# Performance work log

Measured on AMD Instinct MI355X. Metric: run time of the kernel, lower is better.

The kernel has to match this reference:

```python
import jax, jax.numpy as jnp
import numpy as np

B, T, H = 1024, 512, 128
TIMESTEPS_PREDICT = 4


def setup_inputs() -> dict:
    key = jax.random.key(0)
    ks = jax.random.split(key, 7)
    s = 1.0 / np.sqrt(H)
    return {
        "x": jax.random.normal(ks[0], (B, T, 1), jnp.float32),
        "hidden": jnp.zeros((B, H), jnp.float32),
        "fc0_w": jax.random.normal(ks[1], (H, 1), jnp.float32) * s,
        "fc0_b": jax.random.normal(ks[2], (H,), jnp.float32) * 0.1,
        "fc_w": jax.random.normal(ks[3], (H, H), jnp.float32) * s,
        "fc_b": jax.random.normal(ks[4], (H,), jnp.float32) * 0.1,
        "dec_w": jax.random.normal(ks[5], (1, H), jnp.float32) * s,
        "dec_b": jax.random.normal(ks[6], (1,), jnp.float32) * 0.1,
    }


def _rnn(x, h, fc0_w, fc0_b, fc_w, fc_b):
    """Vanilla tanh RNN over time. x: (B, Tx, 1), h: (B, H) -> (ys (B, Tx, H), h)."""
    def step(h, xt):  # xt: (B, 1)
        h = jnp.tanh(xt @ fc0_w.T + fc0_b + h @ fc_w.T + fc_b)
        return h, h
    h, ys = jax.lax.scan(step, h, jnp.swapaxes(x, 0, 1))  # ys: (Tx, B, H)
    return jnp.swapaxes(ys, 0, 1), h


def reference(x, hidden, fc0_w, fc0_b, fc_w, fc_b, dec_w, dec_b):
    out, h = _rnn(x, hidden, fc0_w, fc0_b, fc_w, fc_b)  # (B, T, H)
    y = out @ dec_w.T + dec_b  # (B, T, 1)
    last = y[:, -1:, :]  # (B, 1, 1)
    for _ in range(TIMESTEPS_PREDICT):
        out_h, h = _rnn(last, h, fc0_w, fc0_b, fc_w, fc_b)
        last = out_h @ dec_w.T + dec_b
        y = jnp.concatenate([y, last], axis=1)
    return y  # (B, T + TIMESTEPS_PREDICT, 1)
```

## Files before the change

### kernel.cpp

```cpp
#include <hip/hip_runtime.h>
#include <hip/hip_bf16.h>


#define BB 1024
#define TT 512
#define HH 128
#define TOUT 516
#define BM 16
#define XSTR 513
#define YSTR 517
#define PQS 36
#define TWOLOG2E 2.885390082f

typedef __attribute__((ext_vector_type(8))) _Float16 f16x8;
typedef __attribute__((ext_vector_type(4))) float f32x4;

#define MFMA16(A_, B_, C_) __builtin_amdgcn_mfma_f32_16x16x32_f16(A_, B_, C_, 0, 0, 0)

__global__ void detect_dtype(const void* w, int* flag) {
    const int lane = threadIdx.x;
    const __hip_bfloat16* p = (const __hip_bfloat16*)w;
    const float v0 = __bfloat162float(p[lane]);
    const float v1 = __bfloat162float(p[64 + lane]);
    const bool bad = !(fabsf(v0) < 100.0f) || !(fabsf(v1) < 100.0f);
    const unsigned long long m = __ballot(bad);
    if (lane == 0) *flag = (__popcll(m) > 4) ? 1 : 0;
}

template <bool F32>
__device__ __forceinline__ float ldg(const void* p, int idx) {
    if (F32) return ((const float*)p)[idx];
    return __bfloat162float(((const __hip_bfloat16*)p)[idx]);
}

__device__ __forceinline__ float red32(const float* pqrow) {
    const f32x4* v = (const f32x4*)pqrow;
    const f32x4 s = ((v[0] + v[1]) + (v[2] + v[3])) + ((v[4] + v[5]) + (v[6] + v[7]));
    return (s[0] + s[1]) + (s[2] + s[3]);
}

#define STEP(T_, CUR_, WRITEY_, DOPQ_, READX_, TAILX_) do {                     \
    f16x8 bfrag[4];                                                             \
    _Pragma("unroll")                                                           \
    for (int kf = 0; kf < 4; ++kf)                                              \
        bfrag[kf] = *(const f16x8*)&hbuf[CUR_][n][((((kf << 2) | q) ^ n) & 15) << 3]; \
    float xnext = 0.0f;                                                         \
    if (READX_) xnext = xs[n][(T_) + 1];                                        \
    float xv;                                                                   \
    if (TAILX_) xv = red32(&pq[((T_) - 1) & 1][n][0]) + dbv;                    \
    else        xv = xpref;                                                     \
    f32x4 acc0, acc1;                                                           \
    _Pragma("unroll")                                                           \
    for (int r = 0; r < 4; ++r) acc0[r] = fmaf(xv, w0v[r], bsum[r]);            \
    acc1 = (f32x4){0.f, 0.f, 0.f, 0.f};                                         \
    acc0 = MFMA16(wa[0], bfrag[0], acc0);                                       \
    acc1 = MFMA16(wa[1], bfrag[1], acc1);                                       \
    acc0 = MFMA16(wa[2], bfrag[2], acc0);                                       \
    acc1 = MFMA16(wa[3], bfrag[3], acc1);                                       \
    if (isw7 && (WRITEY_)) {               \
        f32x4 aD0 = (f32x4){0.f, 0.f, 0.f, 0.f};                                \
        f32x4 aD1 = (f32x4){0.f, 0.f, 0.f, 0.f};                                \
        aD0 = MFMA16(wa_d[0], bfrag[0], aD0);                                   \
        aD1 = MFMA16(wa_d[1], bfrag[1], aD1);                                   \
        aD0 = MFMA16(wa_d[2], bfrag[2], aD0);                                   \
        aD1 = MFMA16(wa_d[3], bfrag[3], aD1);                                   \
        const float yp = aD0[0] + aD1[0] + dbv;                                 \
        if (q == 0) ybuf[n][(T_) - 1] = yp;                                     \
    }                                                                           \
    float zs[4], ex[4], rc[4], hv[4];                                           \
    _Pragma("unroll")                                                           \
    for (int r = 0; r < 4; ++r) zs[r] = acc0[r] + acc1[r];                      \
    _Pragma("unroll")                                                           \
    for (int r = 0; r < 4; ++r) ex[r] = __builtin_amdgcn_exp2f(zs[r]);          \
    _Pragma("unroll")                                                           \
    for (int r = 0; r < 4; ++r) rc[r] = __builtin_amdgcn_rcpf(ex[r] + 1.0f);    \
    _Pragma("unroll")                                                           \
    for (int r = 0; r < 4; ++r) hv[r] = fmaf(-2.0f, rc[r], 1.0f);               \
    float p = 0.0f;                                                             \
    if (DOPQ_) {                                                                \
        _Pragma("unroll")                                                       \
        for (int r = 0; r < 4; ++r) p = fmaf(decv[r], hv[r], p);                \
    }                                                                           \
    uint2 pk;                                                                   \
    pk.x = __builtin_bit_cast(unsigned, __builtin_amdgcn_cvt_pkrtz(hv[0], hv[1])); \
    pk.y = __builtin_bit_cast(unsigned, __builtin_amdgcn_cvt_pkrtz(hv[2], hv[3])); \
    *(uint2*)&hbuf[(CUR_) ^ 1][n][((((2 * wv + (q >> 1)) ^ n) & 15) << 3) + ((q & 1) << 2)] = pk; \
    if (DOPQ_) pq[(T_) & 1][n][wv * 4 + q] = p;                                 \
    if (READX_) xpref = xnext;                                                  \
    __syncthreads();                                                            \
} while (0)

template <bool F32>
__device__ void rnn_body(const void* __restrict__ xg, const void* __restrict__ h0,
                         const void* __restrict__ w0, const void* __restrict__ b0,
                         const void* __restrict__ W,  const void* __restrict__ bw,
                         const void* __restrict__ dw, const void* __restrict__ db,
                         void* __restrict__ out,
                         float (*xs)[XSTR], float (*ybuf)[YSTR],
                         _Float16 (*hbuf)[BM][HH], float (*pq)[BM][PQS])
{
    const int tid  = threadIdx.x;
    const int lane = tid & 63;
    const int wv   = tid >> 6;
    const int q    = lane >> 4;
    const int n    = lane & 15;
    const int row0 = blockIdx.x * BM;
    const bool isw7 = (wv == 7);

    for (int idx = tid; idx < BM * TT; idx += 512) {
        const int rr = idx >> 9, t2 = idx & (TT - 1);
        xs[rr][t2] = ldg<F32>(xg, (row0 + rr) * TT + t2);
    }
    for (int idx = tid; idx < BM * HH; idx += 512) {
        const int rr = idx >> 7, ii = idx & (HH - 1);
        const int po = ((((ii >> 3) ^ rr) & 15) << 3) + (ii & 7);
        hbuf[0][rr][po] = (_Float16)ldg<F32>(h0, (row0 + rr) * HH + ii);
    }

    f16x8 wa[4];
    {
        const int ia = wv * 16 + n;
        #pragma unroll
        for (int kf = 0; kf < 4; ++kf) {
            const int kb = kf * 32 + q * 8;
            f16x8 fr;
            #pragma unroll
            for (int j = 0; j < 8; ++j)
                fr[j] = (_Float16)(TWOLOG2E * ldg<F32>(W, ia * HH + kb + j));
            wa[kf] = fr;
        }
    }
    f16x8 wa_d[4] = {};
    if (isw7) {
        #pragma unroll
        for (int kf = 0; kf < 4; ++kf) {
            const int kb = kf * 32 + q * 8;
            f16x8 fr = {};
            if (n == 0) {
                #pragma unroll
                for (int j = 0; j < 8; ++j) fr[j] = (_Float16)ldg<F32>(dw, kb + j);
            }
            wa_d[kf] = fr;
        }
    }
    float bsum[4], w0v[4], decv[4];
    #pragma unroll
    for (int r = 0; r < 4; ++r) {
        const int ic = wv * 16 + q * 4 + r;
        bsum[r] = TWOLOG2E * (ldg<F32>(b0, ic) + ldg<F32>(bw, ic));
        w0v[r]  = TWOLOG2E * ldg<F32>(w0, ic);
        decv[r] = ldg<F32>(dw, ic);
    }
    const float dbv = ldg<F32>(db, 0);

    __syncthreads();

    float xpref = xs[n][0];

    STEP(0, 0, false, false, true, false);

    #pragma unroll 1
    for (int t = 1; t < 511; t += 2) {
        STEP(t,     1, true, false, true, false);
        STEP(t + 1, 0, true, false, true, false);
    }

    STEP(511, 1, true, true, false, false);

    #pragma unroll 1
    for (int t = 512; t < 516; ++t) {
        STEP(t, t & 1, true, true, false, true);
    }

    if (isw7 && q == 0)
        ybuf[n][TOUT - 1] = red32(&pq[(TOUT - 1) & 1][n][0]) + dbv;
    __syncthreads();

    for (int rr = 0; rr < BM; ++rr)
        for (int t2 = tid; t2 < TOUT; t2 += 512) {
            const int o = (row0 + rr) * TOUT + t2;
            const float y = ybuf[rr][t2];
            if (F32) ((float*)out)[o] = y;
            else     ((__hip_bfloat16*)out)[o] = __float2bfloat16(y);
        }
}

__global__ __launch_bounds__(512, 2)
void rnn_mfma(const void* __restrict__ xg, const void* __restrict__ h0,
              const void* __restrict__ w0, const void* __restrict__ b0,
              const void* __restrict__ W,  const void* __restrict__ bw,
              const void* __restrict__ dw, const void* __restrict__ db,
              void* __restrict__ out, const int* __restrict__ flag)
{
    __shared__ float xs[BM][XSTR];
    __shared__ float ybuf[BM][YSTR];
    __shared__ __align__(16) _Float16 hbuf[2][BM][HH];
    __shared__ __align__(16) float pq[2][BM][PQS];

    const int f = *(volatile const int*)flag;
    if (f) rnn_body<true >(xg, h0, w0, b0, W, bw, dw, db, out, xs, ybuf, hbuf, pq);
    else   rnn_body<false>(xg, h0, w0, b0, W, bw, dw, db, out, xs, ybuf, hbuf, pq);
}

extern "C" void kernel_launch(void* const* d_in, const int* in_sizes, int n_in,
                              void* d_out, int out_size, void* d_ws, size_t ws_size,
                              hipStream_t stream) {
    int* flag = (int*)d_ws;
    detect_dtype<<<1, 64, 0, stream>>>(d_in[4], flag);
    rnn_mfma<<<BB / BM, 512, 0, stream>>>(d_in[0], d_in[1], d_in[2], d_in[3],
                                          d_in[4], d_in[5], d_in[6], d_in[7],
                                          d_out, flag);
}
```

Baseline: 215.0 us.

## Run each 16-row RNN block in a single wavefront with register-resident hidden state

Each block shrinks from 8 waves to one 64-thread wave. That wave holds all of W in registers as 32 MFMA A-fragments. Hidden units are permuted so the MFMA output fragments map directly onto the next step's B operand, so the hidden state never goes through LDS and the per-step __syncthreads disappears. The decoder dot product is done with two cross-lane shuffles, and outputs go straight to global memory. The cost is that only 64 waves run on the whole GPU, so each serial step's 32 dependent MFMAs plus transcendentals sit on one wave's critical path, and register pressure rises sharply.

Result: slower. 566.4 us (+163.4%).

```diff
diff --git a/kernel.cpp b/kernel.cpp
--- a/kernel.cpp
+++ b/kernel.cpp
@@ -7,13 +7,11 @@
 #define HH 128
 #define TOUT 516
 #define BM 16
-#define XSTR 513
-#define YSTR 517
-#define PQS 36
 #define TWOLOG2E 2.885390082f
 
 typedef __attribute__((ext_vector_type(8))) _Float16 f16x8;
 typedef __attribute__((ext_vector_type(4))) float f32x4;
+typedef __attribute__((ext_vector_type(4))) unsigned int u32x4;
 
 #define MFMA16(A_, B_, C_) __builtin_amdgcn_mfma_f32_16x16x32_f16(A_, B_, C_, 0, 0, 0)
 
@@ -33,173 +31,141 @@
     return __bfloat162float(((const __hip_bfloat16*)p)[idx]);
 }
 
-__device__ __forceinline__ float red32(const float* pqrow) {
-    const f32x4* v = (const f32x4*)pqrow;
-    const f32x4 s = ((v[0] + v[1]) + (v[2] + v[3])) + ((v[4] + v[5]) + (v[6] + v[7]));
-    return (s[0] + s[1]) + (s[2] + s[3]);
+template <bool F32>
+__device__ __forceinline__ void stg(void* p, int idx, float v) {
+    if (F32) ((float*)p)[idx] = v;
+    else     ((__hip_bfloat16*)p)[idx] = __float2bfloat16(v);
 }
 
-#define STEP(T_, CUR_, WRITEY_, DOPQ_, READX_, TAILX_) do {                     \
-    f16x8 bfrag[4];                                                             \
-    _Pragma("unroll")                                                           \
-    for (int kf = 0; kf < 4; ++kf)                                              \
-        bfrag[kf] = *(const f16x8*)&hbuf[CUR_][n][((((kf << 2) | q) ^ n) & 15) << 3]; \
-    float xnext = 0.0f;                                                         \
-    if (READX_) xnext = xs[n][(T_) + 1];                                        \
-    float xv;                                                                   \
-    if (TAILX_) xv = red32(&pq[((T_) - 1) & 1][n][0]) + dbv;                    \
-    else        xv = xpref;                                                     \
-    f32x4 acc0, acc1;                                                           \
-    _Pragma("unroll")                                                           \
-    for (int r = 0; r < 4; ++r) acc0[r] = fmaf(xv, w0v[r], bsum[r]);            \
-    acc1 = (f32x4){0.f, 0.f, 0.f, 0.f};                                         \
-    acc0 = MFMA16(wa[0], bfrag[0], acc0);                                       \
-    acc1 = MFMA16(wa[1], bfrag[1], acc1);                                       \
-    acc0 = MFMA16(wa[2], bfrag[2], acc0);                                       \
-    acc1 = MFMA16(wa[3], bfrag[3], acc1);                                       \
-    if (isw7 && (WRITEY_)) {               \
-        f32x4 aD0 = (f32x4){0.f, 0.f, 0.f, 0.f};                                \
-        f32x4 aD1 = (f32x4){0.f, 0.f, 0.f, 0.f};                                \
-        aD0 = MFMA16(wa_d[0], bfrag[0], aD0);                                   \
-        aD1 = MFMA16(wa_d[1], bfrag[1], aD1);                                   \
-        aD0 = MFMA16(wa_d[2], bfrag[2], aD0);                                   \
-        aD1 = MFMA16(wa_d[3], bfrag[3], aD1);                                   \
-        const float yp = aD0[0] + aD1[0] + dbv;                                 \
-        if (q == 0) ybuf[n][(T_) - 1] = yp;                                     \
-    }                                                                           \
-    float zs[4], ex[4], rc[4], hv[4];                                           \
-    _Pragma("unroll")                                                           \
-    for (int r = 0; r < 4; ++r) zs[r] = acc0[r] + acc1[r];                      \
-    _Pragma("unroll")                                                           \
-    for (int r = 0; r < 4; ++r) ex[r] = __builtin_amdgcn_exp2f(zs[r]);          \
-    _Pragma("unroll")                                                           \
-    for (int r = 0; r < 4; ++r) rc[r] = __builtin_amdgcn_rcpf(ex[r] + 1.0f);    \
-    _Pragma("unroll")                                                           \
-    for (int r = 0; r < 4; ++r) hv[r] = fmaf(-2.0f, rc[r], 1.0f);               \
-    float p = 0.0f;                                                             \
-    if (DOPQ_) {                                                                \
-        _Pragma("unroll")                                                       \
-        for (int r = 0; r < 4; ++r) p = fmaf(decv[r], hv[r], p);                \
-    }                                                                           \
-    uint2 pk;                                                                   \
-    pk.x = __builtin_bit_cast(unsigned, __builtin_amdgcn_cvt_pkrtz(hv[0], hv[1])); \
-    pk.y = __builtin_bit_cast(unsigned, __builtin_amdgcn_cvt_pkrtz(hv[2], hv[3])); \
-    *(uint2*)&hbuf[(CUR_) ^ 1][n][((((2 * wv + (q >> 1)) ^ n) & 15) << 3) + ((q & 1) << 2)] = pk; \
-    if (DOPQ_) pq[(T_) & 1][n][wv * 4 + q] = p;                                 \
-    if (READX_) xpref = xnext;                                                  \
-    __syncthreads();                                                            \
-} while (0)
+__device__ __forceinline__ int unit_of(int mt, int m) {
+    return 32 * (mt & 3) + 8 * (m >> 2) + 4 * (mt >> 2) + (m & 3);
+}
 
 template <bool F32>
 __device__ void rnn_body(const void* __restrict__ xg, const void* __restrict__ h0,
                          const void* __restrict__ w0, const void* __restrict__ b0,
                          const void* __restrict__ W,  const void* __restrict__ bw,
                          const void* __restrict__ dw, const void* __restrict__ db,
-                         void* __restrict__ out,
-                         float (*xs)[XSTR], float (*ybuf)[YSTR],
-                         _Float16 (*hbuf)[BM][HH], float (*pq)[BM][PQS])
+                         void* __restrict__ out, float (*xs)[TT])
 {
     const int tid  = threadIdx.x;
-    const int lane = tid & 63;
-    const int wv   = tid >> 6;
-    const int q    = lane >> 4;
-    const int n    = lane & 15;
+    const int q    = tid >> 4;
+    const int n    = tid & 15;
     const int row0 = blockIdx.x * BM;
-    const bool isw7 = (wv == 7);
 
-    for (int idx = tid; idx < BM * TT; idx += 512) {
+    for (int idx = tid; idx < BM * TT; idx += 64) {
         const int rr = idx >> 9, t2 = idx & (TT - 1);
         xs[rr][t2] = ldg<F32>(xg, (row0 + rr) * TT + t2);
     }
-    for (int idx = tid; idx < BM * HH; idx += 512) {
-        const int rr = idx >> 7, ii = idx & (HH - 1);
-        const int po = ((((ii >> 3) ^ rr) & 15) << 3) + (ii & 7);
-        hbuf[0][rr][po] = (_Float16)ldg<F32>(h0, (row0 + rr) * HH + ii);
-    }
 
-    f16x8 wa[4];
-    {
-        const int ia = wv * 16 + n;
+    f16x8 wa[8][4];
+    #pragma unroll
+    for (int mt = 0; mt < 8; ++mt) {
+        const int row = unit_of(mt, n);
         #pragma unroll
         for (int kf = 0; kf < 4; ++kf) {
-            const int kb = kf * 32 + q * 8;
             f16x8 fr;
             #pragma unroll
             for (int j = 0; j < 8; ++j)
-                fr[j] = (_Float16)(TWOLOG2E * ldg<F32>(W, ia * HH + kb + j));
-            wa[kf] = fr;
+                fr[j] = (_Float16)(TWOLOG2E * ldg<F32>(W, row * HH + 32 * kf + 8 * q + j));
+            wa[mt][kf] = fr;
         }
     }
-    f16x8 wa_d[4] = {};
-    if (isw7) {
+
+    f32x4 bsum[8], w0v[8], decv[8];
+    #pragma unroll
+    for (int mt = 0; mt < 8; ++mt) {
         #pragma unroll
-        for (int kf = 0; kf < 4; ++kf) {
-            const int kb = kf * 32 + q * 8;
-            f16x8 fr = {};
-            if (n == 0) {
-                #pragma unroll
-                for (int j = 0; j < 8; ++j) fr[j] = (_Float16)ldg<F32>(dw, kb + j);
-            }
-            wa_d[kf] = fr;
+        for (int r = 0; r < 4; ++r) {
+            const int u = unit_of(mt, 4 * q + r);
+            bsum[mt][r] = TWOLOG2E * (ldg<F32>(b0, u) + ldg<F32>(bw, u));
+            w0v[mt][r]  = TWOLOG2E * ldg<F32>(w0, u);
+            decv[mt][r] = ldg<F32>(dw, u);
         }
-    }
-    float bsum[4], w0v[4], decv[4];
-    #pragma unroll
-    for (int r = 0; r < 4; ++r) {
-        const int ic = wv * 16 + q * 4 + r;
-        bsum[r] = TWOLOG2E * (ldg<F32>(b0, ic) + ldg<F32>(bw, ic));
-        w0v[r]  = TWOLOG2E * ldg<F32>(w0, ic);
-        decv[r] = ldg<F32>(dw, ic);
     }
     const float dbv = ldg<F32>(db, 0);
 
-    __syncthreads();
+    f16x8 bfr[4];
+    #pragma unroll
+    for (int kf = 0; kf < 4; ++kf) {
+        f16x8 fr;
+        #pragma unroll
+        for (int j = 0; j < 8; ++j)
+            fr[j] = (_Float16)ldg<F32>(h0, (row0 + n) * HH + 32 * kf + 8 * q + j);
+        bfr[kf] = fr;
+    }
 
-    float xpref = xs[n][0];
-
-    STEP(0, 0, false, false, true, false);
+    const int obase = (row0 + n) * TOUT;
+    float xv = xs[n][0];
 
     #pragma unroll 1
-    for (int t = 1; t < 511; t += 2) {
-        STEP(t,     1, true, false, true, false);
-        STEP(t + 1, 0, true, false, true, false);
+    for (int t = 0; t < TOUT; ++t) {
+        f32x4 acc[8];
+        #pragma unroll
+        for (int mt = 0; mt < 8; ++mt) {
+            #pragma unroll
+            for (int r = 0; r < 4; ++r)
+                acc[mt][r] = fmaf(xv, w0v[mt][r], bsum[mt][r]);
+        }
+        #pragma unroll
+        for (int kf = 0; kf < 4; ++kf) {
+            #pragma unroll
+            for (int mt = 0; mt < 8; ++mt)
+                acc[mt] = MFMA16(wa[mt][kf], bfr[kf], acc[mt]);
+        }
+        float xnext = 0.0f;
+        if (t < 511) xnext = xs[n][t + 1];
+        f32x4 ex[8], rc[8], hv[8];
+        #pragma unroll
+        for (int mt = 0; mt < 8; ++mt) {
+            #pragma unroll
+            for (int r = 0; r < 4; ++r) ex[mt][r] = __builtin_amdgcn_exp2f(acc[mt][r]);
+        }
+        #pragma unroll
+        for (int mt = 0; mt < 8; ++mt) {
+            #pragma unroll
+            for (int r = 0; r < 4; ++r) rc[mt][r] = __builtin_amdgcn_rcpf(ex[mt][r] + 1.0f);
+        }
+        #pragma unroll
+        for (int mt = 0; mt < 8; ++mt) {
+            #pragma unroll
+            for (int r = 0; r < 4; ++r) hv[mt][r] = fmaf(-2.0f, rc[mt][r], 1.0f);
+        }
+        float p = 0.0f;
+        #pragma unroll
+        for (int mt = 0; mt < 8; ++mt) {
+            #pragma unroll
+            for (int r = 0; r < 4; ++r) p = fmaf(decv[mt][r], hv[mt][r], p);
+        }
+        p += __shfl_xor(p, 16);
+        p += __shfl_xor(p, 32);
+        const float y = p + dbv;
+        if (q == 0) stg<F32>(out, obase + t, y);
+        #pragma unroll
+        for (int kf = 0; kf < 4; ++kf) {
+            u32x4 w;
+            w[0] = __builtin_bit_cast(unsigned, __builtin_amdgcn_cvt_pkrtz(hv[kf][0], hv[kf][1]));
+            w[1] = __builtin_bit_cast(unsigned, __builtin_amdgcn_cvt_pkrtz(hv[kf][2], hv[kf][3]));
+            w[2] = __builtin_bit_cast(unsigned, __builtin_amdgcn_cvt_pkrtz(hv[kf + 4][0], hv[kf + 4][1]));
+            w[3] = __builtin_bit_cast(unsigned, __builtin_amdgcn_cvt_pkrtz(hv[kf + 4][2], hv[kf + 4][3]));
+            bfr[kf] = __builtin_bit_cast(f16x8, w);
+        }
+        xv = (t < 511) ? xnext : y;
     }
-
-    STEP(511, 1, true, true, false, false);
-
-    #pragma unroll 1
-    for (int t = 512; t < 516; ++t) {
-        STEP(t, t & 1, true, true, false, true);
-    }
-
-    if (isw7 && q == 0)
-        ybuf[n][TOUT - 1] = red32(&pq[(TOUT - 1) & 1][n][0]) + dbv;
-    __syncthreads();
-
-    for (int rr = 0; rr < BM; ++rr)
-        for (int t2 = tid; t2 < TOUT; t2 += 512) {
-            const int o = (row0 + rr) * TOUT + t2;
-            const float y = ybuf[rr][t2];
-            if (F32) ((float*)out)[o] = y;
-            else     ((__hip_bfloat16*)out)[o] = __float2bfloat16(y);
-        }
 }
 
-__global__ __launch_bounds__(512, 2)
+__global__ __launch_bounds__(64, 1)
 void rnn_mfma(const void* __restrict__ xg, const void* __restrict__ h0,
               const void* __restrict__ w0, const void* __restrict__ b0,
               const void* __restrict__ W,  const void* __restrict__ bw,
               const void* __restrict__ dw, const void* __restrict__ db,
               void* __restrict__ out, const int* __restrict__ flag)
 {
-    __shared__ float xs[BM][XSTR];
-    __shared__ float ybuf[BM][YSTR];
-    __shared__ __align__(16) _Float16 hbuf[2][BM][HH];
-    __shared__ __align__(16) float pq[2][BM][PQS];
+    __shared__ float xs[BM][TT];
 
     const int f = *(volatile const int*)flag;
-    if (f) rnn_body<true >(xg, h0, w0, b0, W, bw, dw, db, out, xs, ybuf, hbuf, pq);
-    else   rnn_body<false>(xg, h0, w0, b0, W, bw, dw, db, out, xs, ybuf, hbuf, pq);
+    if (f) rnn_body<true >(xg, h0, w0, b0, W, bw, dw, db, out, xs);
+    else   rnn_body<false>(xg, h0, w0, b0, W, bw, dw, db, out, xs);
 }
 
 extern "C" void kernel_launch(void* const* d_in, const int* in_sizes, int n_in,
@@ -207,7 +173,7 @@
                               hipStream_t stream) {
     int* flag = (int*)d_ws;
     detect_dtype<<<1, 64, 0, stream>>>(d_in[4], flag);
-    rnn_mfma<<<BB / BM, 512, 0, stream>>>(d_in[0], d_in[1], d_in[2], d_in[3],
-                                          d_in[4], d_in[5], d_in[6], d_in[7],
-                                          d_out, flag);
+    rnn_mfma<<<BB / BM, 64, 0, stream>>>(d_in[0], d_in[1], d_in[2], d_in[3],
+                                         d_in[4], d_in[5], d_in[6], d_in[7],
+                                         d_out, flag);
 }
```
